# Performance work log

Measured on AMD Instinct MI355X. Metric: run time of the kernel, lower is better.

## Reference

```python
import jax, jax.numpy as jnp
import numpy as np

ENT = 16
INNER = 64
NEG = 1e12

def _rope_sin_cos(seq_len, dim, dtype):
    # interleaved sinusoidal: pos_emb[s] = [sin0, cos0, sin1, cos1, ...]
    pos = jnp.arange(seq_len, dtype=jnp.float32)[:, None]          # [S,1]
    freqs = jnp.power(10000.0, -2.0 * jnp.arange(dim // 2, dtype=jnp.float32) / dim)
    ang = pos * freqs                                              # [S,D/2]
    sin = jnp.repeat(jnp.sin(ang), 2, axis=-1).astype(dtype)       # [S,D] (each value doubled)
    cos = jnp.repeat(jnp.cos(ang), 2, axis=-1).astype(dtype)       # [S,D]
    return sin[None, :, None, :], cos[None, :, None, :]            # broadcast to [B,S,E,D]

def _rotate_half_interleaved(x):
    # stack([-x[...,1::2], x[...,0::2]], -1).reshape(x.shape)
    return jnp.stack([-x[..., 1::2], x[..., 0::2]], axis=-1).reshape(x.shape)

def setup_inputs() -> dict:
    key = jax.random.key(0)
    k1, k2 = jax.random.split(key)
    B, S, H = 4, 1024, 1024
    last_hidden_state = jax.random.normal(k1, (B, S, H), dtype=jnp.float32)
    W_dense = jax.random.normal(k2, (H, ENT * INNER * 2), dtype=jnp.float32) * (1.0 / np.sqrt(H))
    b_dense = jnp.zeros((ENT * INNER * 2,), dtype=jnp.float32)
    token_lengh = jnp.ones((B, S), dtype=jnp.float32)  # 0/1 padding mask over key positions
    return {"last_hidden_state": last_hidden_state, "W_dense": W_dense,
            "b_dense": b_dense, "token_lengh": token_lengh}

def reference(last_hidden_state, W_dense, b_dense, token_lengh):
    B, S, H = last_hidden_state.shape
    # dense -> [B,S,E,2D]; split into q,k heads per entity type
    out = (last_hidden_state @ W_dense + b_dense).reshape(B, S, ENT, 2 * INNER)
    qw, kw = out[..., :INNER], out[..., INNER:]
    # inline RoPE
    sin, cos = _rope_sin_cos(S, INNER, qw.dtype)
    qw = qw * cos + _rotate_half_interleaved(qw) * sin
    kw = kw * cos + _rotate_half_interleaved(kw) * sin
    # pairwise biaffine scores per entity type
    logits = jnp.einsum('bmhd,bnhd->bhmn', qw, kw)                 # [B,E,S,S]
    # padding mask (key dim only, matching the torch expand semantics)
    pad = token_lengh[:, None, None, :]                            # [B,1,1,S]
    logits = logits * pad - (1.0 - pad) * NEG
    # strict lower-triangular mask (spans with end < start are invalid)
    tril = jnp.tril(jnp.ones((S, S), dtype=logits.dtype), -1)
    logits = logits - tril * NEG
    return logits / jnp.sqrt(jnp.asarray(INNER, dtype=logits.dtype))
```

## Files before the change

### kernel.cpp

```cpp
#include <hip/hip_runtime.h>
#include <hip/hip_bf16.h>
#include <stdint.h>

#define B_   4
#define S_   1024
#define H_   1024
#define NH_  16
#define D_   64
#define N1_  2048
#define M1_  4096
#define NEG_ 1000000000000.0f

typedef __attribute__((ext_vector_type(8))) short bf16x8;
typedef __attribute__((ext_vector_type(4))) float f32x4;

__device__ inline void gload_lds16(const void* g, void* l) {
  __builtin_amdgcn_global_load_lds(
      (const __attribute__((address_space(1))) unsigned int*)g,
      (__attribute__((address_space(3))) unsigned int*)l, 16, 0, 0);
}

__device__ inline unsigned short f2bf(float f) {
  union { float f; uint32_t u; } a; a.f = f;
  uint32_t r = a.u + 0x7fff + ((a.u >> 16) & 1);
  return (unsigned short)(r >> 16);
}


__global__ void k_cast(const float4* __restrict__ in, unsigned short* __restrict__ out, int n4) {
  int i = blockIdx.x * 256 + threadIdx.x;
  if (i >= n4) return;
  float4 v = in[i];
  uint64_t pk = (uint64_t)f2bf(v.x) | ((uint64_t)f2bf(v.y) << 16) |
                ((uint64_t)f2bf(v.z) << 32) | ((uint64_t)f2bf(v.w) << 48);
  ((uint64_t*)out)[i] = pk;
}

__global__ void k_transW(const float* __restrict__ W, unsigned short* __restrict__ WT) {
  __shared__ float t[32][33];
  int nb = blockIdx.x * 32, kb = blockIdx.y * 32;
  int tx = threadIdx.x, ty = threadIdx.y;
  for (int r = 0; r < 4; r++)
    t[ty + r * 8][tx] = W[(size_t)(kb + ty + r * 8) * N1_ + nb + tx];
  __syncthreads();
  for (int r = 0; r < 4; r++)
    WT[(size_t)(nb + ty + r * 8) * H_ + kb + tx] = f2bf(t[tx][ty + r * 8]);
}

__global__ void k_sincos(float* __restrict__ tab) {
  int i = blockIdx.x * 256 + threadIdx.x;
  if (i >= S_ * 32) return;
  int pos = i >> 5, fi = i & 31;
  float freq = exp2f(-(float)fi * (13.2877123795494f / 32.0f));
  float ang = (float)pos * freq;
  tab[2 * i]     = sinf(ang);
  tab[2 * i + 1] = cosf(ang);
}


__global__ __launch_bounds__(256) void k_gemm1(
    const unsigned short* __restrict__ A,
    const unsigned short* __restrict__ BT,
    const float* __restrict__ bias,
    const float* __restrict__ sc,
    unsigned short* __restrict__ qws,
    unsigned short* __restrict__ kws) {
  __shared__ unsigned short a_lds[128 * 32];
  __shared__ unsigned short b_lds[128 * 32];
  int t = threadIdx.x;
  int lane = t & 63, wv = t >> 6;
  int wm = wv >> 1, wn = wv & 1;
  int col = lane & 15, quad = lane >> 4;
  int mBase = blockIdx.y * 128, nBase = blockIdx.x * 128;

  f32x4 acc[4][4] = {};

  for (int kk = 0; kk < H_; kk += 32) {
    for (int c = 0; c < 2; c++) {
      int idx = c * 256 + t;
      int r = idx >> 2, ch = idx & 3;
      gload_lds16(A + (size_t)(mBase + r) * H_ + kk + ch * 8, a_lds + idx * 8);
      gload_lds16(BT + (size_t)(nBase + r) * H_ + kk + ch * 8, b_lds + idx * 8);
    }
    __syncthreads();
    bf16x8 af[4], bf[4];
#pragma unroll
    for (int i = 0; i < 4; i++)
      af[i] = *(const bf16x8*)&a_lds[(wm * 64 + i * 16 + col) * 32 + quad * 8];
#pragma unroll
    for (int j = 0; j < 4; j++)
      bf[j] = *(const bf16x8*)&b_lds[(wn * 64 + j * 16 + col) * 32 + quad * 8];
#pragma unroll
    for (int j = 0; j < 4; j++)
#pragma unroll
      for (int i = 0; i < 4; i++)
        acc[j][i] = __builtin_amdgcn_mfma_f32_16x16x32_bf16(bf[j], af[i], acc[j][i], 0, 0, 0);
    __syncthreads();
  }

#pragma unroll
  for (int i = 0; i < 4; i++) {
    int m = mBase + wm * 64 + i * 16 + col;
    int pos = m & (S_ - 1);
    int bb = m >> 10;
#pragma unroll
    for (int j = 0; j < 4; j++) {
      int n = nBase + wn * 64 + j * 16 + quad * 4;
      int d = n & 63;
      int head = n >> 7;
      int isK = (n >> 6) & 1;
      float4 bj  = *(const float4*)&bias[n];
      float4 scv = *(const float4*)&sc[(pos * 32 + (d >> 1)) * 2];
      float v0 = acc[j][i][0] + bj.x;
      float v1 = acc[j][i][1] + bj.y;
      float v2 = acc[j][i][2] + bj.z;
      float v3 = acc[j][i][3] + bj.w;
      float o0 = v0 * scv.y - v1 * scv.x;
      float o1 = v1 * scv.y + v0 * scv.x;
      float o2 = v2 * scv.w - v3 * scv.z;
      float o3 = v3 * scv.w + v2 * scv.z;
      unsigned short* dst = isK ? kws : qws;
      ushort4 pk;
      pk.x = f2bf(o0); pk.y = f2bf(o1); pk.z = f2bf(o2); pk.w = f2bf(o3);
      *(ushort4*)&dst[((size_t)(bb * NH_ + head) * S_ + pos) * D_ + d] = pk;
    }
  }
}


#define STG_ 132

__global__ __launch_bounds__(256) void k_gemm2(
    const unsigned short* __restrict__ qws,
    const unsigned short* __restrict__ kws,
    const float* __restrict__ tl,
    float* __restrict__ out) {
  __shared__ __align__(16) char smem[64 * STG_ * 4];
  unsigned short* q_lds = (unsigned short*)smem;
  unsigned short* k_lds = q_lds + 128 * 64;
  float* stage = (float*)smem;

  int t = threadIdx.x;
  int lane = t & 63, wv = t >> 6, wm = wv >> 1, wn = wv & 1;
  int col = lane & 15, quad = lane >> 4;
  int z = blockIdx.z;
  int mT = blockIdx.y * 128, nT = blockIdx.x * 128;
  const unsigned short* qb = qws + ((size_t)z * S_ + mT) * D_;
  const unsigned short* kb = kws + ((size_t)z * S_ + nT) * D_;

  for (int c = 0; c < 4; c++) {
    int idx = c * 256 + t;
    gload_lds16(qb + idx * 8, q_lds + idx * 8);
    gload_lds16(kb + idx * 8, k_lds + idx * 8);
  }
  __syncthreads();

  f32x4 acc[4][4] = {};
#pragma unroll
  for (int kk = 0; kk < 64; kk += 32) {
    bf16x8 qf[4], kf[4];
#pragma unroll
    for (int i = 0; i < 4; i++)
      qf[i] = *(const bf16x8*)&q_lds[(wm * 64 + i * 16 + col) * 64 + kk + quad * 8];
#pragma unroll
    for (int j = 0; j < 4; j++)
      kf[j] = *(const bf16x8*)&k_lds[(wn * 64 + j * 16 + col) * 64 + kk + quad * 8];
#pragma unroll
    for (int j = 0; j < 4; j++)
#pragma unroll
      for (int i = 0; i < 4; i++)
        acc[j][i] = __builtin_amdgcn_mfma_f32_16x16x32_bf16(kf[j], qf[i], acc[j][i], 0, 0, 0);
  }
  __syncthreads();

  int bb = z >> 4;
#pragma unroll
  for (int half = 0; half < 2; half++) {
    if (wm == half) {
#pragma unroll
      for (int i = 0; i < 4; i++) {
        int rloc = i * 16 + col;
#pragma unroll
        for (int j = 0; j < 4; j++) {
          int cloc = wn * 64 + j * 16 + quad * 4;
          float4 v;
          v.x = acc[j][i][0]; v.y = acc[j][i][1];
          v.z = acc[j][i][2]; v.w = acc[j][i][3];
          *(float4*)&stage[rloc * STG_ + cloc] = v;
        }
      }
    }
    __syncthreads();
    int mbase = mT + half * 64;
#pragma unroll
    for (int r = 0; r < 8; r++) {
      int f = r * 256 + t;
      int rloc = f >> 5;
      int c4 = (f & 31) * 4;
      float4 v = *(const float4*)&stage[rloc * STG_ + c4];
      int m = mbase + rloc;
      int n = nT + c4;
      float4 pad4 = *(const float4*)&tl[bb * S_ + n];
      float4 o;
      float x;
      x = v.x * pad4.x - (1.0f - pad4.x) * NEG_; if (m > n)     x -= NEG_; o.x = x * 0.125f;
      x = v.y * pad4.y - (1.0f - pad4.y) * NEG_; if (m > n + 1) x -= NEG_; o.y = x * 0.125f;
      x = v.z * pad4.z - (1.0f - pad4.z) * NEG_; if (m > n + 2) x -= NEG_; o.z = x * 0.125f;
      x = v.w * pad4.w - (1.0f - pad4.w) * NEG_; if (m > n + 3) x -= NEG_; o.w = x * 0.125f;
      *(float4*)&out[((size_t)z * S_ + m) * S_ + n] = o;
    }
    __syncthreads();
  }
}


extern "C" void kernel_launch(void* const* d_in, const int* in_sizes, int n_in,
                              void* d_out, int out_size, void* d_ws, size_t ws_size,
                              hipStream_t stream) {
  const float* lhs  = (const float*)d_in[0];
  const float* W    = (const float*)d_in[1];
  const float* bias = (const float*)d_in[2];
  const float* tl   = (const float*)d_in[3];
  float* out = (float*)d_out;

  char* ws = (char*)d_ws;
  unsigned short* lhsb = (unsigned short*)(ws);
  unsigned short* WT   = (unsigned short*)(ws + (8u  << 20));
  unsigned short* qws  = (unsigned short*)(ws + (12u << 20));
  unsigned short* kws  = (unsigned short*)(ws + (20u << 20));
  float*          sc   = (float*)        (ws + (28u << 20));

  k_cast<<<(M1_ * H_ / 4 + 255) / 256, 256, 0, stream>>>((const float4*)lhs, lhsb, M1_ * H_ / 4);
  k_transW<<<dim3(N1_ / 32, H_ / 32), dim3(32, 8), 0, stream>>>(W, WT);
  k_sincos<<<(S_ * 32 + 255) / 256, 256, 0, stream>>>(sc);
  k_gemm1<<<dim3(N1_ / 128, M1_ / 128), 256, 0, stream>>>(lhsb, WT, bias, sc, qws, kws);
  k_gemm2<<<dim3(S_ / 128, S_ / 128, B_ * NH_), 256, 0, stream>>>(qws, kws, tl, out);
}
```

Measured before the change: 341.1 us.

## Merge prep kernels, remap blocks to XCDs, use nontemporal output stores

Folds the cast, weight-transpose and sin/cos table kernels into a single launch that branches on block index, cutting launch overhead. Both GEMMs switch to a 1D grid with a block-to-tile mapping so that blocks landing on the same XCD share A rows (gemm1) or the same batch-head slice (gemm2), improving L2 reuse. The 256MB logits output is written with nontemporal stores to avoid polluting the caches. The mappings hardcode the grid shapes and assume round-robin dispatch of blocks across 8 XCDs.

```diff
diff --git a/kernel.cpp b/kernel.cpp
--- a/kernel.cpp
+++ b/kernel.cpp
@@ -27,34 +27,35 @@
 }
 
 
-__global__ void k_cast(const float4* __restrict__ in, unsigned short* __restrict__ out, int n4) {
-  int i = blockIdx.x * 256 + threadIdx.x;
-  if (i >= n4) return;
-  float4 v = in[i];
-  uint64_t pk = (uint64_t)f2bf(v.x) | ((uint64_t)f2bf(v.y) << 16) |
-                ((uint64_t)f2bf(v.z) << 32) | ((uint64_t)f2bf(v.w) << 48);
-  ((uint64_t*)out)[i] = pk;
-}
-
-__global__ void k_transW(const float* __restrict__ W, unsigned short* __restrict__ WT) {
-  __shared__ float t[32][33];
-  int nb = blockIdx.x * 32, kb = blockIdx.y * 32;
-  int tx = threadIdx.x, ty = threadIdx.y;
-  for (int r = 0; r < 4; r++)
-    t[ty + r * 8][tx] = W[(size_t)(kb + ty + r * 8) * N1_ + nb + tx];
-  __syncthreads();
-  for (int r = 0; r < 4; r++)
-    WT[(size_t)(nb + ty + r * 8) * H_ + kb + tx] = f2bf(t[tx][ty + r * 8]);
-}
-
-__global__ void k_sincos(float* __restrict__ tab) {
-  int i = blockIdx.x * 256 + threadIdx.x;
-  if (i >= S_ * 32) return;
-  int pos = i >> 5, fi = i & 31;
-  float freq = exp2f(-(float)fi * (13.2877123795494f / 32.0f));
-  float ang = (float)pos * freq;
-  tab[2 * i]     = sinf(ang);
-  tab[2 * i + 1] = cosf(ang);
+__global__ __launch_bounds__(256) void k_prep(
+    const float4* __restrict__ lhs4, unsigned short* __restrict__ lhsb,
+    const float* __restrict__ W, unsigned short* __restrict__ WT,
+    float* __restrict__ tab) {
+  __shared__ float tsm[32][33];
+  int b = blockIdx.x, t = threadIdx.x;
+  if (b < 4096) {
+    int i = b * 256 + t;
+    float4 v = lhs4[i];
+    uint64_t pk = (uint64_t)f2bf(v.x) | ((uint64_t)f2bf(v.y) << 16) |
+                  ((uint64_t)f2bf(v.z) << 32) | ((uint64_t)f2bf(v.w) << 48);
+    ((uint64_t*)lhsb)[i] = pk;
+  } else if (b < 6144) {
+    int bb = b - 4096;
+    int nb = (bb & 63) * 32, kb = (bb >> 6) * 32;
+    int tx = t & 31, ty = t >> 5;
+    for (int r = 0; r < 4; r++)
+      tsm[ty + r * 8][tx] = W[(size_t)(kb + ty + r * 8) * N1_ + nb + tx];
+    __syncthreads();
+    for (int r = 0; r < 4; r++)
+      WT[(size_t)(nb + ty + r * 8) * H_ + kb + tx] = f2bf(tsm[tx][ty + r * 8]);
+  } else {
+    int i = (b - 6144) * 256 + t;
+    int pos = i >> 5, fi = i & 31;
+    float freq = exp2f(-(float)fi * (13.2877123795494f / 32.0f));
+    float ang = (float)pos * freq;
+    tab[2 * i]     = sinf(ang);
+    tab[2 * i + 1] = cosf(ang);
+  }
 }
 
 
@@ -71,7 +72,11 @@
   int lane = t & 63, wv = t >> 6;
   int wm = wv >> 1, wn = wv & 1;
   int col = lane & 15, quad = lane >> 4;
-  int mBase = blockIdx.y * 128, nBase = blockIdx.x * 128;
+
+  int l = blockIdx.x;
+  int xcd = l & 7, k = l >> 3;
+  int mBase = (((k & 3) << 3) + xcd) * 128;
+  int nBase = (k >> 2) * 128;
 
   f32x4 acc[4][4] = {};
 
@@ -143,8 +148,13 @@
   int t = threadIdx.x;
   int lane = t & 63, wv = t >> 6, wm = wv >> 1, wn = wv & 1;
   int col = lane & 15, quad = lane >> 4;
-  int z = blockIdx.z;
-  int mT = blockIdx.y * 128, nT = blockIdx.x * 128;
+
+  int l = blockIdx.x;
+  int xcd = l & 7, k = l >> 3;
+  int z = (xcd << 3) + (k >> 6);
+  int tile = k & 63;
+  int mT = (tile >> 3) * 128, nT = (tile & 7) * 128;
+
   const unsigned short* qb = qws + ((size_t)z * S_ + mT) * D_;
   const unsigned short* kb = kws + ((size_t)z * S_ + nT) * D_;
 
@@ -201,13 +211,13 @@
       int m = mbase + rloc;
       int n = nT + c4;
       float4 pad4 = *(const float4*)&tl[bb * S_ + n];
-      float4 o;
+      f32x4 o;
       float x;
       x = v.x * pad4.x - (1.0f - pad4.x) * NEG_; if (m > n)     x -= NEG_; o.x = x * 0.125f;
       x = v.y * pad4.y - (1.0f - pad4.y) * NEG_; if (m > n + 1) x -= NEG_; o.y = x * 0.125f;
       x = v.z * pad4.z - (1.0f - pad4.z) * NEG_; if (m > n + 2) x -= NEG_; o.z = x * 0.125f;
       x = v.w * pad4.w - (1.0f - pad4.w) * NEG_; if (m > n + 3) x -= NEG_; o.w = x * 0.125f;
-      *(float4*)&out[((size_t)z * S_ + m) * S_ + n] = o;
+      __builtin_nontemporal_store(o, (f32x4*)&out[((size_t)z * S_ + m) * S_ + n]);
     }
     __syncthreads();
   }
@@ -230,9 +240,7 @@
   unsigned short* kws  = (unsigned short*)(ws + (20u << 20));
   float*          sc   = (float*)        (ws + (28u << 20));
 
-  k_cast<<<(M1_ * H_ / 4 + 255) / 256, 256, 0, stream>>>((const float4*)lhs, lhsb, M1_ * H_ / 4);
-  k_transW<<<dim3(N1_ / 32, H_ / 32), dim3(32, 8), 0, stream>>>(W, WT);
-  k_sincos<<<(S_ * 32 + 255) / 256, 256, 0, stream>>>(sc);
-  k_gemm1<<<dim3(N1_ / 128, M1_ / 128), 256, 0, stream>>>(lhsb, WT, bias, sc, qws, kws);
-  k_gemm2<<<dim3(S_ / 128, S_ / 128, B_ * NH_), 256, 0, stream>>>(qws, kws, tl, out);
-}
+  k_prep<<<6272, 256, 0, stream>>>((const float4*)lhs, lhsb, W, WT, sc);
+  k_gemm1<<<512, 256, 0, stream>>>(lhsb, WT, bias, sc, qws, kws);
+  k_gemm2<<<4096, 256, 0, stream>>>(qws, kws, tl, out);
+}
```

Result: faster. 315.9 us (-7.4%).
